# Kernel optimization log

Measured on AMD Instinct MI355X. Metric: run time of the kernel, lower is better.

The kernel has to match this reference:

```python
import jax, jax.numpy as jnp
import numpy as np

B, S, H = 1, 2048, 4096
NH, NKV, HD = 32, 8, 128
GROUP = 128
NEG = jnp.float32(-1e9)


def setup_inputs() -> dict:
    key = jax.random.key(0)
    ks = jax.random.split(key, 13)
    inp = {"hidden_states": jax.random.normal(ks[0], (B, S, H), dtype=jnp.float32)}

    def qparams(k1, k2, k3, out_dim, in_dim):
        qw = jax.random.randint(k1, (out_dim, in_dim), 0, 16, dtype=jnp.int32)
        sc = jax.random.uniform(k2, (out_dim, in_dim // GROUP), dtype=jnp.float32) * 0.02 + 0.001
        zp = jax.random.randint(k3, (out_dim, in_dim // GROUP), 0, 16, dtype=jnp.int32)
        return qw, sc, zp

    inp["q_qw"], inp["q_sc"], inp["q_zp"] = qparams(ks[1], ks[2], ks[3], NH * HD, H)
    inp["k_qw"], inp["k_sc"], inp["k_zp"] = qparams(ks[4], ks[5], ks[6], NKV * HD, H)
    inp["v_qw"], inp["v_sc"], inp["v_zp"] = qparams(ks[7], ks[8], ks[9], NKV * HD, H)
    inp["o_qw"], inp["o_sc"], inp["o_zp"] = qparams(ks[10], ks[11], ks[12], NH * HD, H)
    return inp


def dequant(qw, sc, zp):
    # W4A16 groupwise dequant: w = (q - zero_point) * scale, group along input dim
    out_dim, in_dim = qw.shape
    g = in_dim // sc.shape[1]
    w = (qw.reshape(out_dim, -1, g) - zp[:, :, None]).astype(jnp.float32) * sc[:, :, None]
    return w.reshape(out_dim, in_dim)


def reference(hidden_states, q_qw, q_sc, q_zp, k_qw, k_sc, k_zp,
              v_qw, v_sc, v_zp, o_qw, o_sc, o_zp):
    x = hidden_states  # [B, S, H]
    grp = NH // NKV  # GQA groups = 4

    q = jnp.einsum('bsh,oh->bso', x, dequant(q_qw, q_sc, q_zp))
    k = jnp.einsum('bsh,oh->bso', x, dequant(k_qw, k_sc, k_zp))
    v = jnp.einsum('bsh,oh->bso', x, dequant(v_qw, v_sc, v_zp))

    # [B, NKV, grp, S, HD] for q; [B, NKV, S, HD] for k, v (avoid repeat_kv materialization)
    q = q.reshape(B, S, NKV, grp, HD).transpose(0, 2, 3, 1, 4)
    k = k.reshape(B, S, NKV, HD).transpose(0, 2, 1, 3)
    v = v.reshape(B, S, NKV, HD).transpose(0, 2, 1, 3)

    scale = 1.0 / jnp.sqrt(jnp.float32(HD))
    scores = jnp.einsum('bngqd,bnkd->bngqk', q, k) * scale  # [B,NKV,grp,S,S]
    causal = jnp.tril(jnp.ones((S, S), dtype=bool))
    scores = jnp.where(causal[None, None, None], scores, NEG)
    probs = jax.nn.softmax(scores, axis=-1)
    attn = jnp.einsum('bngqk,bnkd->bngqd', probs, v)  # [B,NKV,grp,S,HD]

    attn = attn.transpose(0, 3, 1, 2, 4).reshape(B, S, NH * HD)
    out = jnp.einsum('bso,ho->bsh', attn, dequant(o_qw, o_sc, o_zp).T.T) if False else jnp.einsum('bsf,of->bso', attn, dequant(o_qw, o_sc, o_zp))
    return out
```

## Files before the change

### kernel.cpp

```cpp
#include <hip/hip_runtime.h>
#include <stdint.h>

#define DI __device__ __forceinline__

typedef __attribute__((ext_vector_type(8))) _Float16 f16x8;
typedef __attribute__((ext_vector_type(4))) float f32x4;
typedef __attribute__((ext_vector_type(4))) int   i32x4;
typedef __attribute__((ext_vector_type(4))) float fvec4;
typedef __attribute__((ext_vector_type(8))) unsigned short u16x8;
typedef __attribute__((ext_vector_type(4))) unsigned short u16x4;

constexpr int S2   = 2048;
constexpr int NHD  = 4096;
constexpr int KVD  = 1024;
constexpr int QKVW = 6144;
constexpr float SCALE_LOG2E = 0.08838834764831845f * 1.4426950408889634f;

DI unsigned short f32_f16(float f) {
    union { _Float16 h; unsigned short u; } v;
    v.h = (_Float16)f;
    return v.u;
}

DI f32x4 mfma16(f16x8 a, f16x8 b, f32x4 c) {
    return __builtin_amdgcn_mfma_f32_16x16x32_f16(a, b, c, 0, 0, 0);
}

DI void load_lds16(const void* g, void* l) {
    __builtin_amdgcn_global_load_lds(
        (const __attribute__((address_space(1))) void*)(uintptr_t)g,
        (__attribute__((address_space(3))) void*)(uintptr_t)l, 16, 0, 0);
}

__global__ __launch_bounds__(256) void k_cast(const float* __restrict__ in,
                                              unsigned short* __restrict__ out) {
    int i = (blockIdx.x * 256 + threadIdx.x) * 4;
    fvec4 v = *(const fvec4*)(in + i);
    u16x4 o;
#pragma unroll
    for (int j = 0; j < 4; ++j) o[j] = f32_f16(v[j]);
    *(u16x4*)(out + i) = o;
}

__global__ __launch_bounds__(256) void k_prep(const int* __restrict__ qw,
                                              const float* __restrict__ sc,
                                              const int* __restrict__ zp,
                                              unsigned short* __restrict__ outW) {
    long long t = (long long)blockIdx.x * 256 + threadIdx.x;
    long long base = t * 8;
    int n = (int)(base >> 12);
    int g = (int)((base >> 7) & 31);
    float s = sc[n * 32 + g];
    int   z = zp[n * 32 + g];
    i32x4 a = *(const i32x4*)(qw + base);
    i32x4 b = *(const i32x4*)(qw + base + 4);
    u16x8 o;
#pragma unroll
    for (int j = 0; j < 4; ++j) {
        o[j]     = f32_f16((float)(a[j] - z) * s);
        o[4 + j] = f32_f16((float)(b[j] - z) * s);
    }
    *(u16x8*)(outW + base) = o;
}

template <typename CT>
__global__ __launch_bounds__(256) void k_gemm(const unsigned short* __restrict__ A,
                                              const unsigned short* __restrict__ B,
                                              CT* __restrict__ C, int N) {
    constexpr int K = 4096;
    __shared__ __align__(16) unsigned short Al[128 * 32];
    __shared__ __align__(16) unsigned short Bl[128 * 32];
    const int m0 = blockIdx.y * 128, n0 = blockIdx.x * 128;
    const int tid = threadIdx.x;
    const int wave = tid >> 6, lane = tid & 63;
    const int wm = wave >> 1, wn = wave & 1;
    const int lq = lane & 15, lg = lane >> 4;
    const int srow = lane >> 2, scol = (lane & 3) * 8;
    f32x4 acc[4][4] = {};

    for (int k0 = 0; k0 < K; k0 += 32) {
        __syncthreads();
#pragma unroll
        for (int it = 0; it < 2; ++it) {
            const int r0 = (wave * 2 + it) * 16;
            load_lds16(A + (long long)(m0 + r0 + srow) * K + k0 + scol, Al + r0 * 32);
            load_lds16(B + (long long)(n0 + r0 + srow) * K + k0 + scol, Bl + r0 * 32);
        }
        __syncthreads();
        f16x8 af[4], bf[4];
#pragma unroll
        for (int i = 0; i < 4; ++i) {
            af[i] = *(const f16x8*)(Al + (wm * 64 + i * 16 + lq) * 32 + lg * 8);
            bf[i] = *(const f16x8*)(Bl + (wn * 64 + i * 16 + lq) * 32 + lg * 8);
        }
#pragma unroll
        for (int mi = 0; mi < 4; ++mi)
#pragma unroll
            for (int ni = 0; ni < 4; ++ni)
                acc[mi][ni] = mfma16(af[mi], bf[ni], acc[mi][ni]);
    }
#pragma unroll
    for (int mi = 0; mi < 4; ++mi)
#pragma unroll
        for (int ni = 0; ni < 4; ++ni)
#pragma unroll
            for (int r = 0; r < 4; ++r) {
                const int row = m0 + wm * 64 + mi * 16 + lg * 4 + r;
                const int col = n0 + wn * 64 + ni * 16 + lq;
                const float v = acc[mi][ni][r];
                if constexpr (sizeof(CT) == 2) C[(long long)row * N + col] = (CT)f32_f16(v);
                else                           C[(long long)row * N + col] = v;
            }
}

__global__ __launch_bounds__(256) void k_transpose_v(const unsigned short* __restrict__ QKV,
                                                     unsigned short* __restrict__ VT) {
    __shared__ unsigned short tile[32][33];
    const int s0 = blockIdx.x * 32, d0 = blockIdx.y * 32, hk = blockIdx.z;
    const int tx = threadIdx.x & 31, ty = threadIdx.x >> 5;
#pragma unroll
    for (int j = 0; j < 4; ++j)
        tile[ty + j * 8][tx] =
            QKV[(long long)(s0 + ty + j * 8) * QKVW + (NHD + KVD) + hk * 128 + d0 + tx];
    __syncthreads();
#pragma unroll
    for (int j = 0; j < 4; ++j)
        VT[((long long)hk * 128 + d0 + ty + j * 8) * S2 + s0 + tx] = tile[tx][ty + j * 8];
}

__global__ __launch_bounds__(256, 4) void k_attn(const unsigned short* __restrict__ QKV,
                                                 const unsigned short* __restrict__ VT,
                                                 unsigned short* __restrict__ O) {
    __shared__ __align__(16) unsigned short Ks[2][32 * 128];
    __shared__ __align__(16) unsigned short Vs[2][128 * 32];
    __shared__ __align__(16) unsigned short Ps[4][16 * 40];
    const int bid = blockIdx.x;
    const int hkv = bid & 7;
    const int tq  = bid >> 3;
    const int g   = (tq < 64) ? tq : 191 - tq;
    const int nt  = (g >> 1) + 1;
    const int q0  = g * 16;
    const int tid = threadIdx.x;
    const int w = tid >> 6, lane = tid & 63;
    const int lq = lane & 15, lg = lane >> 4;
    const int h = hkv * 4 + w;

    const unsigned short* Kg  = QKV + NHD + hkv * 128;
    const unsigned short* VTg = VT + (long long)hkv * 128 * S2;

    const int ksr = lane >> 4;
    const int ksc = lane & 15;
    const int vsr = lane >> 2;
    const int vsc = lane & 3;
    const int vsx = (lane >> 3) & 3;

    f16x8 qf[4];
    const unsigned short* qp = QKV + (long long)(q0 + lq) * QKVW + h * 128;
#pragma unroll
    for (int kc = 0; kc < 4; ++kc) qf[kc] = *(const f16x8*)(qp + kc * 32 + lg * 8);

    f32x4 oacc[8] = {};
    float m[4], l[4];
#pragma unroll
    for (int r = 0; r < 4; ++r) { m[r] = -1e30f; l[r] = 0.f; }

    auto stage = [&](int j0, int b) {
#pragma unroll
        for (int i = 0; i < 2; ++i) {
            const int r = 8 * w + 4 * i + ksr;
            load_lds16(Kg + (long long)(j0 + r) * QKVW + ((ksc ^ (r & 7)) << 3),
                       &Ks[b][(8 * w + 4 * i) * 128]);
        }
#pragma unroll
        for (int i = 0; i < 2; ++i) {
            const int r = 32 * w + 16 * i + vsr;
            load_lds16(VTg + (long long)r * S2 + j0 + ((vsc ^ vsx) << 3),
                       &Vs[b][(32 * w + 16 * i) * 32]);
        }
    };

    stage(0, 0);
    int buf = 0;
    for (int t = 0; t < nt; ++t) {
        const int j0 = t * 32;
        __syncthreads();
        if (t + 1 < nt) stage(j0 + 32, buf ^ 1);

        f32x4 sv[2] = {};
        __builtin_amdgcn_s_setprio(1);
#pragma unroll
        for (int kc = 0; kc < 4; ++kc)
#pragma unroll
            for (int jj = 0; jj < 2; ++jj) {
                const int c = (kc * 4 + lg) ^ (lq & 7);
                f16x8 kf = *(const f16x8*)&Ks[buf][(jj * 16 + lq) * 128 + c * 8];
                sv[jj] = mfma16(qf[kc], kf, sv[jj]);
            }
        __builtin_amdgcn_s_setprio(0);

        float t0a[4], t1a[4], pl[4];
        const bool diag = (t == nt - 1);
#pragma unroll
        for (int r = 0; r < 4; ++r) {
            float t0 = sv[0][r] * SCALE_LOG2E;
            float t1 = sv[1][r] * SCALE_LOG2E;
            if (diag) {
                const int qg = q0 + lg * 4 + r;
                if (j0 + lq > qg)      t0 = -INFINITY;
                if (j0 + 16 + lq > qg) t1 = -INFINITY;
            }
            t0a[r] = t0; t1a[r] = t1;
            pl[r] = fmaxf(t0, t1);
        }
        const bool grow = (pl[0] > m[0] + 8.f) || (pl[1] > m[1] + 8.f) ||
                          (pl[2] > m[2] + 8.f) || (pl[3] > m[3] + 8.f);
        if (__any(grow)) {
#pragma unroll
            for (int r = 0; r < 4; ++r) {
                float mx = pl[r];
                mx = fmaxf(mx, __shfl_xor(mx, 1));
                mx = fmaxf(mx, __shfl_xor(mx, 2));
                mx = fmaxf(mx, __shfl_xor(mx, 4));
                mx = fmaxf(mx, __shfl_xor(mx, 8));
                const float mn = fmaxf(m[r], mx);
                const float alpha = exp2f(m[r] - mn);
                m[r] = mn;
                l[r] *= alpha;
#pragma unroll
                for (int nb = 0; nb < 8; ++nb) oacc[nb][r] *= alpha;
            }
        }
#pragma unroll
        for (int r = 0; r < 4; ++r) {
            const float p0 = exp2f(t0a[r] - m[r]);
            const float p1 = exp2f(t1a[r] - m[r]);
            l[r] += p0 + p1;
            Ps[w][(lg * 4 + r) * 40 + lq]      = f32_f16(p0);
            Ps[w][(lg * 4 + r) * 40 + 16 + lq] = f32_f16(p1);
        }
        const f16x8 pf = *(const f16x8*)&Ps[w][lq * 40 + lg * 8];
        __builtin_amdgcn_s_setprio(1);
#pragma unroll
        for (int nb = 0; nb < 8; ++nb) {
            const int c = lg ^ ((lq >> 1) & 3);
            f16x8 vf = *(const f16x8*)&Vs[buf][(nb * 16 + lq) * 32 + c * 8];
            oacc[nb] = mfma16(pf, vf, oacc[nb]);
        }
        __builtin_amdgcn_s_setprio(0);
        buf ^= 1;
    }

    float linv[4];
#pragma unroll
    for (int r = 0; r < 4; ++r) {
        float s = l[r];
        s += __shfl_xor(s, 1);
        s += __shfl_xor(s, 2);
        s += __shfl_xor(s, 4);
        s += __shfl_xor(s, 8);
        linv[r] = 1.0f / s;
    }
#pragma unroll
    for (int nb = 0; nb < 8; ++nb)
#pragma unroll
        for (int r = 0; r < 4; ++r) {
            const int row = q0 + lg * 4 + r;
            const int col = h * 128 + nb * 16 + lq;
            O[(long long)row * NHD + col] = f32_f16(oacc[nb][r] * linv[r]);
        }
}

extern "C" void kernel_launch(void* const* d_in, const int* in_sizes, int n_in,
                              void* d_out, int out_size, void* d_ws, size_t ws_size,
                              hipStream_t stream) {
    (void)in_sizes; (void)n_in; (void)out_size; (void)ws_size;
    const float* hs  = (const float*)d_in[0];
    const int*   qqw = (const int*)d_in[1];
    const float* qsc = (const float*)d_in[2];
    const int*   qzp = (const int*)d_in[3];
    const int*   kqw = (const int*)d_in[4];
    const float* ksc = (const float*)d_in[5];
    const int*   kzp = (const int*)d_in[6];
    const int*   vqw = (const int*)d_in[7];
    const float* vsc = (const float*)d_in[8];
    const int*   vzp = (const int*)d_in[9];
    const int*   oqw = (const int*)d_in[10];
    const float* osc = (const float*)d_in[11];
    const int*   ozp = (const int*)d_in[12];

    char* ws = (char*)d_ws;
    unsigned short* x16  = (unsigned short*)(ws);
    unsigned short* wbuf = (unsigned short*)(ws + (16ULL << 20));
    unsigned short* vt   = (unsigned short*)(ws + (65ULL << 20));
    unsigned short* xatt = (unsigned short*)(ws + (69ULL << 20));
    unsigned short* qkv  = (unsigned short*)d_out;
    float* out = (float*)d_out;

    k_cast<<<8192, 256, 0, stream>>>(hs, x16);
    k_prep<<<8192, 256, 0, stream>>>(qqw, qsc, qzp, wbuf);
    k_prep<<<2048, 256, 0, stream>>>(kqw, ksc, kzp, wbuf + (size_t)4096 * 4096);
    k_prep<<<2048, 256, 0, stream>>>(vqw, vsc, vzp, wbuf + (size_t)5120 * 4096);
    k_gemm<unsigned short><<<dim3(48, 16), 256, 0, stream>>>(x16, wbuf, qkv, QKVW);
    k_transpose_v<<<dim3(64, 4, 8), 256, 0, stream>>>(qkv, vt);
    k_prep<<<8192, 256, 0, stream>>>(oqw, osc, ozp, wbuf);
    k_attn<<<1024, 256, 0, stream>>>(qkv, vt, xatt);
    k_gemm<float><<<dim3(32, 16), 256, 0, stream>>>(xatt, wbuf, out, 4096);
}
```

Measured before the change: 357.2 us.

## Double-buffer GEMM LDS tiles with async prefetch and XOR-swizzled layout

The GEMM main loop now keeps two LDS buffers and issues the direct-to-LDS global loads for the next K tile before computing the current one. It waits with manual vmcnt counts and raw s_barrier instead of __syncthreads. LDS columns are XOR-swizzled on both the store and read side to cut bank conflicts, and MFMA issue gets a raised wave priority. The goal is to hide global load latency and LDS conflicts, at the cost of double the LDS footprint and fragile hand-written waitcnt assumptions.

```diff
diff --git a/kernel.cpp b/kernel.cpp
--- a/kernel.cpp
+++ b/kernel.cpp
@@ -68,36 +68,56 @@
                                               const unsigned short* __restrict__ B,
                                               CT* __restrict__ C, int N) {
     constexpr int K = 4096;
-    __shared__ __align__(16) unsigned short Al[128 * 32];
-    __shared__ __align__(16) unsigned short Bl[128 * 32];
+    constexpr int NT = K / 32;
+    __shared__ __align__(16) unsigned short Al[2][128 * 32];
+    __shared__ __align__(16) unsigned short Bl[2][128 * 32];
     const int m0 = blockIdx.y * 128, n0 = blockIdx.x * 128;
     const int tid = threadIdx.x;
     const int wave = tid >> 6, lane = tid & 63;
     const int wm = wave >> 1, wn = wave & 1;
     const int lq = lane & 15, lg = lane >> 4;
-    const int srow = lane >> 2, scol = (lane & 3) * 8;
+    const int srow = lane >> 2;
+    const int scol = (((lane & 3) ^ ((srow >> 1) & 3)) << 3);
+    const int cx   = ((lg ^ ((lq >> 1) & 3)) << 3);
     f32x4 acc[4][4] = {};
 
-    for (int k0 = 0; k0 < K; k0 += 32) {
-        __syncthreads();
+    auto stage = [&](int k0, int b) {
 #pragma unroll
         for (int it = 0; it < 2; ++it) {
             const int r0 = (wave * 2 + it) * 16;
-            load_lds16(A + (long long)(m0 + r0 + srow) * K + k0 + scol, Al + r0 * 32);
-            load_lds16(B + (long long)(n0 + r0 + srow) * K + k0 + scol, Bl + r0 * 32);
-        }
-        __syncthreads();
+            load_lds16(A + (long long)(m0 + r0 + srow) * K + k0 + scol, &Al[b][r0 * 32]);
+            load_lds16(B + (long long)(n0 + r0 + srow) * K + k0 + scol, &Bl[b][r0 * 32]);
+        }
+    };
+
+    stage(0, 0);
+    int buf = 0;
+    for (int t = 0; t < NT; ++t) {
+        if (t + 1 < NT) {
+            stage((t + 1) * 32, buf ^ 1);
+            asm volatile("s_waitcnt vmcnt(4)" ::: "memory");
+        } else {
+            asm volatile("s_waitcnt vmcnt(0)" ::: "memory");
+        }
+        __builtin_amdgcn_s_barrier();
+        __builtin_amdgcn_sched_barrier(0);
         f16x8 af[4], bf[4];
 #pragma unroll
         for (int i = 0; i < 4; ++i) {
-            af[i] = *(const f16x8*)(Al + (wm * 64 + i * 16 + lq) * 32 + lg * 8);
-            bf[i] = *(const f16x8*)(Bl + (wn * 64 + i * 16 + lq) * 32 + lg * 8);
-        }
+            af[i] = *(const f16x8*)(&Al[buf][(wm * 64 + i * 16 + lq) * 32 + cx]);
+            bf[i] = *(const f16x8*)(&Bl[buf][(wn * 64 + i * 16 + lq) * 32 + cx]);
+        }
+        __builtin_amdgcn_s_setprio(1);
 #pragma unroll
         for (int mi = 0; mi < 4; ++mi)
 #pragma unroll
             for (int ni = 0; ni < 4; ++ni)
                 acc[mi][ni] = mfma16(af[mi], bf[ni], acc[mi][ni]);
+        __builtin_amdgcn_s_setprio(0);
+        __builtin_amdgcn_sched_barrier(0);
+        __builtin_amdgcn_s_barrier();
+        __builtin_amdgcn_sched_barrier(0);
+        buf ^= 1;
     }
 #pragma unroll
     for (int mi = 0; mi < 4; ++mi)
```

Result: faster. 342.5 us (-4.1%).

## Triple-buffer GEMM LDS loads with swizzle, tile remap, and MFMA priority

Applied to the files above, without the earlier changes.

The projection GEMM now keeps three LDS stages, prefetching two K-tiles ahead and waiting on vmcnt instead of using two full __syncthreads per iteration. It also XOR-swizzles the LDS layout to reduce bank conflicts, remaps block IDs so that consecutive blocks spread across tiles for better cache locality, and splits the A fragment loads so they interleave with MFMA groups under s_setprio. The intent is to overlap global loads with compute. In exchange it uses more LDS per block (launch_bounds 256,3) and relies on careful hand-written waitcnt ordering.

```diff
diff --git a/kernel.cpp b/kernel.cpp
--- a/kernel.cpp
+++ b/kernel.cpp
@@ -64,40 +64,74 @@
 }
 
 template <typename CT>
-__global__ __launch_bounds__(256) void k_gemm(const unsigned short* __restrict__ A,
-                                              const unsigned short* __restrict__ B,
-                                              CT* __restrict__ C, int N) {
-    constexpr int K = 4096;
-    __shared__ __align__(16) unsigned short Al[128 * 32];
-    __shared__ __align__(16) unsigned short Bl[128 * 32];
-    const int m0 = blockIdx.y * 128, n0 = blockIdx.x * 128;
+__global__ __launch_bounds__(256, 3) void k_gemm(const unsigned short* __restrict__ A,
+                                                 const unsigned short* __restrict__ B,
+                                                 CT* __restrict__ C, int N) {
+    constexpr int K = 4096, BK = 32, NT = K / BK;
+    __shared__ __align__(16) unsigned short Al[3][128 * 32];
+    __shared__ __align__(16) unsigned short Bl[3][128 * 32];
+    const int nbx = N / 128;
+    const int tot = nbx * (int)gridDim.y;
+    const int hg  = (int)blockIdx.x + (int)blockIdx.y * nbx;
+    const int lid = (hg & 7) * (tot >> 3) + (hg >> 3);
+    const int m0 = (lid / nbx) * 128, n0 = (lid % nbx) * 128;
     const int tid = threadIdx.x;
     const int wave = tid >> 6, lane = tid & 63;
     const int wm = wave >> 1, wn = wave & 1;
     const int lq = lane & 15, lg = lane >> 4;
-    const int srow = lane >> 2, scol = (lane & 3) * 8;
+    const int cx = (lg ^ ((lq >> 1) & 3)) << 3;
+    const int srow = lane >> 2;
+    const int gc = (((lane & 3) ^ ((lane >> 3) & 3)) << 3);
     f32x4 acc[4][4] = {};
 
-    for (int k0 = 0; k0 < K; k0 += 32) {
-        __syncthreads();
+    auto stage = [&](int k0, int sl) {
 #pragma unroll
         for (int it = 0; it < 2; ++it) {
             const int r0 = (wave * 2 + it) * 16;
-            load_lds16(A + (long long)(m0 + r0 + srow) * K + k0 + scol, Al + r0 * 32);
-            load_lds16(B + (long long)(n0 + r0 + srow) * K + k0 + scol, Bl + r0 * 32);
-        }
-        __syncthreads();
+            load_lds16(A + (long long)(m0 + r0 + srow) * K + k0 + gc, &Al[sl][r0 * 32]);
+            load_lds16(B + (long long)(n0 + r0 + srow) * K + k0 + gc, &Bl[sl][r0 * 32]);
+        }
+    };
+
+    stage(0, 0);
+    stage(BK, 1);
+    int cs = 0, ss = 2;
+    for (int kt = 0; kt < NT; ++kt) {
+        if (kt < NT - 1) asm volatile("s_waitcnt vmcnt(4)" ::: "memory");
+        else             asm volatile("s_waitcnt vmcnt(0)" ::: "memory");
+        __builtin_amdgcn_s_barrier();
+        __builtin_amdgcn_sched_barrier(0);
+        if (kt + 2 < NT) stage((kt + 2) * BK, ss);
         f16x8 af[4], bf[4];
 #pragma unroll
-        for (int i = 0; i < 4; ++i) {
-            af[i] = *(const f16x8*)(Al + (wm * 64 + i * 16 + lq) * 32 + lg * 8);
-            bf[i] = *(const f16x8*)(Bl + (wn * 64 + i * 16 + lq) * 32 + lg * 8);
-        }
-#pragma unroll
-        for (int mi = 0; mi < 4; ++mi)
+        for (int i = 0; i < 4; ++i)
+            bf[i] = *(const f16x8*)(&Bl[cs][(wn * 64 + i * 16 + lq) * 32 + cx]);
+#pragma unroll
+        for (int i = 0; i < 2; ++i)
+            af[i] = *(const f16x8*)(&Al[cs][(wm * 64 + i * 16 + lq) * 32 + cx]);
+        __builtin_amdgcn_sched_barrier(0);
+        __builtin_amdgcn_s_setprio(1);
+#pragma unroll
+        for (int mi = 0; mi < 2; ++mi)
 #pragma unroll
             for (int ni = 0; ni < 4; ++ni)
                 acc[mi][ni] = mfma16(af[mi], bf[ni], acc[mi][ni]);
+        __builtin_amdgcn_s_setprio(0);
+        __builtin_amdgcn_sched_barrier(0);
+#pragma unroll
+        for (int i = 2; i < 4; ++i)
+            af[i] = *(const f16x8*)(&Al[cs][(wm * 64 + i * 16 + lq) * 32 + cx]);
+        __builtin_amdgcn_sched_barrier(0);
+        __builtin_amdgcn_s_setprio(1);
+#pragma unroll
+        for (int mi = 2; mi < 4; ++mi)
+#pragma unroll
+            for (int ni = 0; ni < 4; ++ni)
+                acc[mi][ni] = mfma16(af[mi], bf[ni], acc[mi][ni]);
+        __builtin_amdgcn_s_setprio(0);
+        __builtin_amdgcn_sched_barrier(0);
+        if (++cs == 3) cs = 0;
+        if (++ss == 3) ss = 0;
     }
 #pragma unroll
     for (int mi = 0; mi < 4; ++mi)
```

New measurement: 358.3 us. About the same (+0.3%).
